# Optimization experiments

Hardware: AMD Instinct MI355X
Metric: run time of the kernel (lower is better)

## Reference

```python
import jax, jax.numpy as jnp
import numpy as np

B, IN_DIM, D, C = 8192, 2048, 1024, 1000


def setup_inputs() -> dict:
    key = jax.random.key(0)
    k1, k2, k3 = jax.random.split(key, 3)
    x = jax.random.normal(k1, (B, IN_DIM), dtype=jnp.float32)
    W_enc = jax.random.normal(k2, (IN_DIM, D), dtype=jnp.float32) * 0.02
    b_enc = jnp.zeros((D,), dtype=jnp.float32)
    prototypes = jax.random.normal(k3, (C, D), dtype=jnp.float32)
    return {"x": x, "W_enc": W_enc, "b_enc": b_enc, "prototypes": prototypes}


def reference(x, W_enc, b_enc, prototypes):
    # Encoder features Z: [B, D] (stand-in for model.forward_encoder)
    Z = x @ W_enc + b_enc
    # MSELoss(Z[i], proto[j]) = mean over D of squared diff
    # = (||z||^2 + ||p||^2 - 2 z.p) / D  -- avoids [B, C, D] intermediate
    z2 = jnp.sum(Z * Z, axis=-1, keepdims=True)          # [B, 1]
    p2 = jnp.sum(prototypes * prototypes, axis=-1)[None]  # [1, C]
    cross = jnp.einsum("bd,cd->bc", Z, prototypes)        # [B, C]
    mse = (z2 + p2 - 2.0 * cross) / jnp.asarray(Z.shape[-1], Z.dtype)
    return -mse
```

## Files before the change

### kernel.cpp

```cpp
#include <hip/hip_runtime.h>

#define B_ROWS 8192
#define IN_DIM 2048
#define D_DIM  1024
#define C_CLS  1000

typedef __attribute__((ext_vector_type(8))) short   bf16x8;
typedef __attribute__((ext_vector_type(4))) float   f32x4;

__device__ __forceinline__ unsigned short f2b(float f) {
    unsigned int u = __builtin_bit_cast(unsigned int, f);
    u = u + 0x7fffu + ((u >> 16) & 1u);
    return (unsigned short)(u >> 16);
}
__device__ __forceinline__ void g2lds16(const void* g, void* l) {
    __builtin_amdgcn_global_load_lds(
        (const __attribute__((address_space(1))) unsigned int*)g,
        (__attribute__((address_space(3))) unsigned int*)l,
        16, 0, 0);
}

__global__ __launch_bounds__(256) void k_pre(const float* __restrict__ W,
                                             const float* __restrict__ P,
                                             const float* __restrict__ x,
                                             unsigned short* __restrict__ Wt,
                                             unsigned short* __restrict__ Pb,
                                             unsigned short* __restrict__ xb,
                                             float* __restrict__ p2) {
    const int tid = threadIdx.x;
    if (blockIdx.x >= 3072) {
        const size_t i = (((size_t)blockIdx.x - 3072) * 256 + tid) * 8;
        float4 v0 = *(const float4*)(x + i);
        float4 v1 = *(const float4*)(x + i + 4);
        bf16x8 h;
        h[0] = (short)f2b(v0.x); h[1] = (short)f2b(v0.y);
        h[2] = (short)f2b(v0.z); h[3] = (short)f2b(v0.w);
        h[4] = (short)f2b(v1.x); h[5] = (short)f2b(v1.y);
        h[6] = (short)f2b(v1.z); h[7] = (short)f2b(v1.w);
        *(bf16x8*)(xb + i) = h;
    } else if (blockIdx.x < 2048) {
        __shared__ float t[32][33];
        const int tx = tid & 31, ty = tid >> 5;
        const int kb = (blockIdx.x & 63) * 32;
        const int nb = (blockIdx.x >> 6) * 32;
#pragma unroll
        for (int j = 0; j < 4; ++j)
            t[ty + 8 * j][tx] = W[(size_t)(kb + ty + 8 * j) * D_DIM + nb + tx];
        __syncthreads();
#pragma unroll
        for (int j = 0; j < 4; ++j)
            Wt[(size_t)(nb + ty + 8 * j) * IN_DIM + kb + tx] = f2b(t[tx][ty + 8 * j]);
    } else {
        const int c = blockIdx.x - 2048;
        float s = 0.f;
        if (c < C_CLS) {
            float4 v = *((const float4*)(P + (size_t)c * D_DIM) + tid);
            s = v.x * v.x + v.y * v.y + v.z * v.z + v.w * v.w;
            ushort4 h; h.x = f2b(v.x); h.y = f2b(v.y); h.z = f2b(v.z); h.w = f2b(v.w);
            *((ushort4*)(Pb + (size_t)c * D_DIM) + tid) = h;
        } else {
            ushort4 h; h.x = 0; h.y = 0; h.z = 0; h.w = 0;
            *((ushort4*)(Pb + (size_t)c * D_DIM) + tid) = h;
        }
#pragma unroll
        for (int o = 32; o > 0; o >>= 1) s += __shfl_down(s, o);
        __shared__ float red[4];
        if ((tid & 63) == 0) red[tid >> 6] = s;
        __syncthreads();
        if (tid == 0) p2[c] = red[0] + red[1] + red[2] + red[3];
    }
}

template <int MODE>
__global__ __launch_bounds__(512, 2) void k_gemm8(
    const unsigned short* __restrict__ Ab,
    const unsigned short* __restrict__ Bt,
    const float* __restrict__ bias,
    const float* __restrict__ z2p_in,
    const float* __restrict__ p2,
    unsigned short* __restrict__ Zout,
    float* __restrict__ z2p_out,
    float* __restrict__ Out) {
    constexpr int K  = (MODE == 0) ? IN_DIM : D_DIM;
    constexpr int NT = K / 64;
    constexpr unsigned ASZ = 256 * 64 * 2;
    constexpr unsigned BSZ = 128 * 64 * 2;
    extern __shared__ char lds[];
    char* pa0 = lds;            char* pa1 = lds + ASZ;  char* pa2 = lds + 2 * ASZ;
    char* pb0 = lds + 3 * ASZ;  char* pb1 = pb0 + BSZ;  char* pb2 = pb0 + 2 * BSZ;
    float* z2loc = (float*)(lds + 3 * (ASZ + BSZ));

    const int tid  = threadIdx.x;
    const int wave = tid >> 6, lane = tid & 63;
    const int lo = lane & 15, hi = lane >> 4;
    const int wm = wave >> 1, wn = wave & 1;

    const int swz = ((blockIdx.x & 7) << 5) + (blockIdx.x >> 3);
    const int bm = swz >> 3, bn = swz & 7;
    const int rowbase = bm * 256, colbase = bn * 128;

    const int srow   = lane >> 3;
    const int gchunk = (lane & 7) ^ (srow & 7);

    auto STAGE_A = [&](char* dst, int kt, int i) {
        const int s = i * 8 + wave;
        g2lds16(Ab + (size_t)(rowbase + s * 8 + srow) * K + kt * 64 + gchunk * 8,
                dst + s * 1024);
    };
    auto STAGE_B = [&](char* dst, int kt, int i) {
        const int s = i * 8 + wave;
        g2lds16(Bt + (size_t)(colbase + s * 8 + srow) * K + kt * 64 + gchunk * 8,
                dst + s * 1024);
    };

    f32x4 acc[4][4];
#pragma unroll
    for (int m = 0; m < 4; ++m)
#pragma unroll
        for (int n = 0; n < 4; ++n) acc[m][n] = (f32x4){0.f, 0.f, 0.f, 0.f};

    if constexpr (MODE == 1) {
        if (tid < 256) {
            float s = 0.f;
#pragma unroll
            for (int j = 0; j < 16; ++j) s += z2p_in[j * B_ROWS + rowbase + tid];
            z2loc[tid] = s;
        }
    }
#pragma unroll
    for (int i = 0; i < 4; ++i) STAGE_A(pa0, 0, i);
    STAGE_B(pb0, 0, 0); STAGE_B(pb0, 0, 1);
#pragma unroll
    for (int i = 0; i < 4; ++i) STAGE_A(pa1, 1, i);
    STAGE_B(pb1, 1, 0); STAGE_B(pb1, 1, 1);
    asm volatile("s_waitcnt vmcnt(6) lgkmcnt(0)" ::: "memory");
    __builtin_amdgcn_s_barrier();

    auto COMPUTE = [&]() {
#pragma unroll
        for (int ks = 0; ks < 2; ++ks) {
            bf16x8 af[4], bfr[4];
#pragma unroll
            for (int m = 0; m < 4; ++m) {
                const int row = wm * 64 + m * 16 + lo;
                unsigned addr = (unsigned)(row * 128 + ks * 64 + hi * 16)
                              ^ (unsigned)((lo & 7) << 4);
                af[m] = *(const bf16x8*)(pa0 + addr);
            }
#pragma unroll
            for (int n = 0; n < 4; ++n) {
                const int row = wn * 64 + n * 16 + lo;
                unsigned addr = (unsigned)(row * 128 + ks * 64 + hi * 16)
                              ^ (unsigned)((lo & 7) << 4);
                bfr[n] = *(const bf16x8*)(pb0 + addr);
            }
            __builtin_amdgcn_s_setprio(1);
#pragma unroll
            for (int m = 0; m < 4; ++m)
#pragma unroll
                for (int n = 0; n < 4; ++n)
                    acc[m][n] = __builtin_amdgcn_mfma_f32_16x16x32_bf16(
                        af[m], bfr[n], acc[m][n], 0, 0, 0);
            __builtin_amdgcn_s_setprio(0);
        }
    };

    for (int t = 0; t < NT; ++t) {
        const bool stg = (t < NT - 2);
        if (stg) {
#pragma unroll
            for (int i = 0; i < 4; ++i) STAGE_A(pa2, t + 2, i);
            STAGE_B(pb2, t + 2, 0); STAGE_B(pb2, t + 2, 1);
        }
        COMPUTE();
        if (t < NT - 1) {
            if (stg) asm volatile("s_waitcnt vmcnt(6)" ::: "memory");
            else     asm volatile("s_waitcnt vmcnt(0)" ::: "memory");
            __builtin_amdgcn_s_barrier();
            char* ta = pa0; pa0 = pa1; pa1 = pa2; pa2 = ta;
            char* tb = pb0; pb0 = pb1; pb1 = pb2; pb2 = tb;
        }
    }

    if constexpr (MODE == 0) {
        float bv[4];
#pragma unroll
        for (int n = 0; n < 4; ++n) bv[n] = bias[colbase + wn * 64 + n * 16 + lo];
#pragma unroll
        for (int m = 0; m < 4; ++m)
#pragma unroll
            for (int r = 0; r < 4; ++r) {
                const int rg = rowbase + wm * 64 + m * 16 + hi * 4 + r;
                float s = 0.f;
#pragma unroll
                for (int n = 0; n < 4; ++n) {
                    const float zf = acc[m][n][r] + bv[n];
                    Zout[(size_t)rg * D_DIM + colbase + wn * 64 + n * 16 + lo] = f2b(zf);
                    s += zf * zf;
                }
                s += __shfl_xor(s, 1); s += __shfl_xor(s, 2);
                s += __shfl_xor(s, 4); s += __shfl_xor(s, 8);
                if (lo == 0) z2p_out[(size_t)(bn * 2 + wn) * B_ROWS + rg] = s;
            }
    } else {
        float p2v[4];
#pragma unroll
        for (int n = 0; n < 4; ++n) p2v[n] = p2[colbase + wn * 64 + n * 16 + lo];
#pragma unroll
        for (int m = 0; m < 4; ++m)
#pragma unroll
            for (int r = 0; r < 4; ++r) {
                const int rl = wm * 64 + m * 16 + hi * 4 + r;
                const int rg = rowbase + rl;
                const float zv = z2loc[rl];
#pragma unroll
                for (int n = 0; n < 4; ++n) {
                    const int cg = colbase + wn * 64 + n * 16 + lo;
                    if (cg < C_CLS)
                        Out[(size_t)rg * C_CLS + cg] =
                            (2.f * acc[m][n][r] - zv - p2v[n]) * (1.f / 1024.f);
                }
            }
    }
}

extern "C" void kernel_launch(void* const* d_in, const int* in_sizes, int n_in,
                              void* d_out, int out_size, void* d_ws, size_t ws_size,
                              hipStream_t stream) {
    const float* x = (const float*)d_in[0];
    const float* W = (const float*)d_in[1];
    const float* b = (const float*)d_in[2];
    const float* P = (const float*)d_in[3];
    float* out = (float*)d_out;

    char* ws = (char*)d_ws;
    unsigned short* Wt  = (unsigned short*)(ws);
    unsigned short* Pb  = (unsigned short*)(ws + (4  << 20));
    unsigned short* Zb  = (unsigned short*)(ws + (6  << 20));
    float*          p2  = (float*)(ws + (22 << 20) + (64 << 10));
    float*          z2p = (float*)(ws + (22 << 20) + (128 << 10));
    unsigned short* xb  = (unsigned short*)(ws + (23 << 20));

    const unsigned lds_bytes = 3 * (256 * 64 * 2 + 128 * 64 * 2) + 1024;

    k_pre<<<dim3(11264), dim3(256), 0, stream>>>(W, P, x, Wt, Pb, xb, p2);
    k_gemm8<0><<<dim3(256), dim3(512), lds_bytes, stream>>>(
        xb, Wt, b, nullptr, nullptr, Zb, z2p, nullptr);
    k_gemm8<1><<<dim3(256), dim3(512), lds_bytes, stream>>>(
        Zb, Pb, nullptr, z2p, p2, nullptr, nullptr, out);
}
```

Baseline: 80.53 us.

## Split MFMA main loop into four quadrant phases interleaving LDS reads and staging

Restructures the per-tile compute loop into four quadrant phases. Each phase reads a small set of A/B fragments from LDS, issues part of the global-to-LDS staging for tile t+2, then runs eight MFMAs. Barriers separate the phases so waves stay in lockstep, in the style of ping-pong scheduling. The aim is to overlap LDS reads and global loads with MFMA issue and to lower register pressure. The cost is several extra barriers per tile, plus some B fragments reloaded from LDS.

```diff
diff --git a/kernel.cpp b/kernel.cpp
--- a/kernel.cpp
+++ b/kernel.cpp
@@ -136,43 +136,88 @@
     asm volatile("s_waitcnt vmcnt(6) lgkmcnt(0)" ::: "memory");
     __builtin_amdgcn_s_barrier();
 
-    auto COMPUTE = [&]() {
-#pragma unroll
-        for (int ks = 0; ks < 2; ++ks) {
-            bf16x8 af[4], bfr[4];
-#pragma unroll
-            for (int m = 0; m < 4; ++m) {
-                const int row = wm * 64 + m * 16 + lo;
-                unsigned addr = (unsigned)(row * 128 + ks * 64 + hi * 16)
-                              ^ (unsigned)((lo & 7) << 4);
-                af[m] = *(const bf16x8*)(pa0 + addr);
-            }
-#pragma unroll
-            for (int n = 0; n < 4; ++n) {
-                const int row = wn * 64 + n * 16 + lo;
-                unsigned addr = (unsigned)(row * 128 + ks * 64 + hi * 16)
-                              ^ (unsigned)((lo & 7) << 4);
-                bfr[n] = *(const bf16x8*)(pb0 + addr);
-            }
-            __builtin_amdgcn_s_setprio(1);
-#pragma unroll
-            for (int m = 0; m < 4; ++m)
-#pragma unroll
-                for (int n = 0; n < 4; ++n)
-                    acc[m][n] = __builtin_amdgcn_mfma_f32_16x16x32_bf16(
-                        af[m], bfr[n], acc[m][n], 0, 0, 0);
-            __builtin_amdgcn_s_setprio(0);
-        }
+    auto RD_A = [&](int mrow, int ks) -> bf16x8 {
+        const int row = wm * 64 + mrow * 16 + lo;
+        unsigned addr = (unsigned)(row * 128 + ks * 64 + hi * 16)
+                      ^ (unsigned)((lo & 7) << 4);
+        return *(const bf16x8*)(pa0 + addr);
+    };
+    auto RD_B = [&](int nrow, int ks) -> bf16x8 {
+        const int row = wn * 64 + nrow * 16 + lo;
+        unsigned addr = (unsigned)(row * 128 + ks * 64 + hi * 16)
+                      ^ (unsigned)((lo & 7) << 4);
+        return *(const bf16x8*)(pb0 + addr);
     };
 
     for (int t = 0; t < NT; ++t) {
         const bool stg = (t < NT - 2);
-        if (stg) {
-#pragma unroll
-            for (int i = 0; i < 4; ++i) STAGE_A(pa2, t + 2, i);
-            STAGE_B(pb2, t + 2, 0); STAGE_B(pb2, t + 2, 1);
-        }
-        COMPUTE();
+        bf16x8 a0k0, a0k1, a1k0, a1k1;
+        bf16x8 b0k0, b0k1, b1k0, b1k1;
+
+        a0k0 = RD_A(0, 0); a0k1 = RD_A(0, 1);
+        a1k0 = RD_A(1, 0); a1k1 = RD_A(1, 1);
+        b0k0 = RD_B(0, 0); b0k1 = RD_B(0, 1);
+        b1k0 = RD_B(1, 0); b1k1 = RD_B(1, 1);
+        if (stg) { STAGE_A(pa2, t + 2, 0); STAGE_A(pa2, t + 2, 1); }
+        __builtin_amdgcn_s_barrier();
+        __builtin_amdgcn_s_setprio(1);
+        acc[0][0] = __builtin_amdgcn_mfma_f32_16x16x32_bf16(a0k0, b0k0, acc[0][0], 0, 0, 0);
+        acc[0][1] = __builtin_amdgcn_mfma_f32_16x16x32_bf16(a0k0, b1k0, acc[0][1], 0, 0, 0);
+        acc[1][0] = __builtin_amdgcn_mfma_f32_16x16x32_bf16(a1k0, b0k0, acc[1][0], 0, 0, 0);
+        acc[1][1] = __builtin_amdgcn_mfma_f32_16x16x32_bf16(a1k0, b1k0, acc[1][1], 0, 0, 0);
+        acc[0][0] = __builtin_amdgcn_mfma_f32_16x16x32_bf16(a0k1, b0k1, acc[0][0], 0, 0, 0);
+        acc[0][1] = __builtin_amdgcn_mfma_f32_16x16x32_bf16(a0k1, b1k1, acc[0][1], 0, 0, 0);
+        acc[1][0] = __builtin_amdgcn_mfma_f32_16x16x32_bf16(a1k1, b0k1, acc[1][0], 0, 0, 0);
+        acc[1][1] = __builtin_amdgcn_mfma_f32_16x16x32_bf16(a1k1, b1k1, acc[1][1], 0, 0, 0);
+        __builtin_amdgcn_s_setprio(0);
+        __builtin_amdgcn_s_barrier();
+
+        b0k0 = RD_B(2, 0); b0k1 = RD_B(2, 1);
+        b1k0 = RD_B(3, 0); b1k1 = RD_B(3, 1);
+        if (stg) { STAGE_A(pa2, t + 2, 2); STAGE_A(pa2, t + 2, 3); }
+        __builtin_amdgcn_s_barrier();
+        __builtin_amdgcn_s_setprio(1);
+        acc[0][2] = __builtin_amdgcn_mfma_f32_16x16x32_bf16(a0k0, b0k0, acc[0][2], 0, 0, 0);
+        acc[0][3] = __builtin_amdgcn_mfma_f32_16x16x32_bf16(a0k0, b1k0, acc[0][3], 0, 0, 0);
+        acc[1][2] = __builtin_amdgcn_mfma_f32_16x16x32_bf16(a1k0, b0k0, acc[1][2], 0, 0, 0);
+        acc[1][3] = __builtin_amdgcn_mfma_f32_16x16x32_bf16(a1k0, b1k0, acc[1][3], 0, 0, 0);
+        acc[0][2] = __builtin_amdgcn_mfma_f32_16x16x32_bf16(a0k1, b0k1, acc[0][2], 0, 0, 0);
+        acc[0][3] = __builtin_amdgcn_mfma_f32_16x16x32_bf16(a0k1, b1k1, acc[0][3], 0, 0, 0);
+        acc[1][2] = __builtin_amdgcn_mfma_f32_16x16x32_bf16(a1k1, b0k1, acc[1][2], 0, 0, 0);
+        acc[1][3] = __builtin_amdgcn_mfma_f32_16x16x32_bf16(a1k1, b1k1, acc[1][3], 0, 0, 0);
+        __builtin_amdgcn_s_setprio(0);
+        __builtin_amdgcn_s_barrier();
+
+        a0k0 = RD_A(2, 0); a0k1 = RD_A(2, 1);
+        a1k0 = RD_A(3, 0); a1k1 = RD_A(3, 1);
+        if (stg) { STAGE_B(pb2, t + 2, 0); STAGE_B(pb2, t + 2, 1); }
+        __builtin_amdgcn_s_barrier();
+        __builtin_amdgcn_s_setprio(1);
+        acc[2][2] = __builtin_amdgcn_mfma_f32_16x16x32_bf16(a0k0, b0k0, acc[2][2], 0, 0, 0);
+        acc[2][3] = __builtin_amdgcn_mfma_f32_16x16x32_bf16(a0k0, b1k0, acc[2][3], 0, 0, 0);
+        acc[3][2] = __builtin_amdgcn_mfma_f32_16x16x32_bf16(a1k0, b0k0, acc[3][2], 0, 0, 0);
+        acc[3][3] = __builtin_amdgcn_mfma_f32_16x16x32_bf16(a1k0, b1k0, acc[3][3], 0, 0, 0);
+        acc[2][2] = __builtin_amdgcn_mfma_f32_16x16x32_bf16(a0k1, b0k1, acc[2][2], 0, 0, 0);
+        acc[2][3] = __builtin_amdgcn_mfma_f32_16x16x32_bf16(a0k1, b1k1, acc[2][3], 0, 0, 0);
+        acc[3][2] = __builtin_amdgcn_mfma_f32_16x16x32_bf16(a1k1, b0k1, acc[3][2], 0, 0, 0);
+        acc[3][3] = __builtin_amdgcn_mfma_f32_16x16x32_bf16(a1k1, b1k1, acc[3][3], 0, 0, 0);
+        __builtin_amdgcn_s_setprio(0);
+        __builtin_amdgcn_s_barrier();
+
+        b0k0 = RD_B(0, 0); b0k1 = RD_B(0, 1);
+        b1k0 = RD_B(1, 0); b1k1 = RD_B(1, 1);
+        __builtin_amdgcn_s_barrier();
+        __builtin_amdgcn_s_setprio(1);
+        acc[2][0] = __builtin_amdgcn_mfma_f32_16x16x32_bf16(a0k0, b0k0, acc[2][0], 0, 0, 0);
+        acc[2][1] = __builtin_amdgcn_mfma_f32_16x16x32_bf16(a0k0, b1k0, acc[2][1], 0, 0, 0);
+        acc[3][0] = __builtin_amdgcn_mfma_f32_16x16x32_bf16(a1k0, b0k0, acc[3][0], 0, 0, 0);
+        acc[3][1] = __builtin_amdgcn_mfma_f32_16x16x32_bf16(a1k0, b1k0, acc[3][1], 0, 0, 0);
+        acc[2][0] = __builtin_amdgcn_mfma_f32_16x16x32_bf16(a0k1, b0k1, acc[2][0], 0, 0, 0);
+        acc[2][1] = __builtin_amdgcn_mfma_f32_16x16x32_bf16(a0k1, b1k1, acc[2][1], 0, 0, 0);
+        acc[3][0] = __builtin_amdgcn_mfma_f32_16x16x32_bf16(a1k1, b0k1, acc[3][0], 0, 0, 0);
+        acc[3][1] = __builtin_amdgcn_mfma_f32_16x16x32_bf16(a1k1, b1k1, acc[3][1], 0, 0, 0);
+        __builtin_amdgcn_s_setprio(0);
+
         if (t < NT - 1) {
             if (stg) asm volatile("s_waitcnt vmcnt(6)" ::: "memory");
             else     asm volatile("s_waitcnt vmcnt(0)" ::: "memory");
```

New measurement: 83.73 us. +4.0%, slower.

## Shrink GEMM block tile to 128x128 with four waves and double buffering

Applied to the files above, without the earlier changes.

Both GEMM kernels move from 256x128 tiles run by 512-thread blocks with a three-stage LDS pipeline to 128x128 tiles run by 256-thread blocks with two-stage buffering. The launch grid doubles to 512 blocks and the LDS footprint per block shrinks. The aim is more blocks in flight per CU and less LDS pressure. In exchange, each tile is reused less, so more global traffic is needed. Each iteration also waits on vmcnt(0), which removes the deeper prefetch overlap.

```diff
diff --git a/kernel.cpp b/kernel.cpp
--- a/kernel.cpp
+++ b/kernel.cpp
@@ -72,7 +72,7 @@
 }
 
 template <int MODE>
-__global__ __launch_bounds__(512, 2) void k_gemm8(
+__global__ __launch_bounds__(256, 2) void k_gemm(
     const unsigned short* __restrict__ Ab,
     const unsigned short* __restrict__ Bt,
     const float* __restrict__ bias,
@@ -83,34 +83,40 @@
     float* __restrict__ Out) {
     constexpr int K  = (MODE == 0) ? IN_DIM : D_DIM;
     constexpr int NT = K / 64;
-    constexpr unsigned ASZ = 256 * 64 * 2;
+    constexpr unsigned ASZ = 128 * 64 * 2;
     constexpr unsigned BSZ = 128 * 64 * 2;
     extern __shared__ char lds[];
-    char* pa0 = lds;            char* pa1 = lds + ASZ;  char* pa2 = lds + 2 * ASZ;
-    char* pb0 = lds + 3 * ASZ;  char* pb1 = pb0 + BSZ;  char* pb2 = pb0 + 2 * BSZ;
-    float* z2loc = (float*)(lds + 3 * (ASZ + BSZ));
+    char* pa0 = lds;             char* pa1 = lds + ASZ;
+    char* pb0 = lds + 2 * ASZ;   char* pb1 = pb0 + BSZ;
+    float* z2loc = (float*)(lds + 2 * ASZ + 2 * BSZ);
 
     const int tid  = threadIdx.x;
     const int wave = tid >> 6, lane = tid & 63;
     const int lo = lane & 15, hi = lane >> 4;
     const int wm = wave >> 1, wn = wave & 1;
 
-    const int swz = ((blockIdx.x & 7) << 5) + (blockIdx.x >> 3);
+    const int swz = (blockIdx.x & 7) * 64 + (blockIdx.x >> 3);
     const int bm = swz >> 3, bn = swz & 7;
-    const int rowbase = bm * 256, colbase = bn * 128;
+    const int rowbase = bm * 128, colbase = bn * 128;
 
     const int srow   = lane >> 3;
     const int gchunk = (lane & 7) ^ (srow & 7);
 
-    auto STAGE_A = [&](char* dst, int kt, int i) {
-        const int s = i * 8 + wave;
-        g2lds16(Ab + (size_t)(rowbase + s * 8 + srow) * K + kt * 64 + gchunk * 8,
-                dst + s * 1024);
+    auto STAGE_A = [&](char* dst, int kt) {
+#pragma unroll
+        for (int i = 0; i < 4; ++i) {
+            const int s = i * 4 + wave;
+            g2lds16(Ab + (size_t)(rowbase + s * 8 + srow) * K + kt * 64 + gchunk * 8,
+                    dst + s * 1024);
+        }
     };
-    auto STAGE_B = [&](char* dst, int kt, int i) {
-        const int s = i * 8 + wave;
-        g2lds16(Bt + (size_t)(colbase + s * 8 + srow) * K + kt * 64 + gchunk * 8,
-                dst + s * 1024);
+    auto STAGE_B = [&](char* dst, int kt) {
+#pragma unroll
+        for (int i = 0; i < 4; ++i) {
+            const int s = i * 4 + wave;
+            g2lds16(Bt + (size_t)(colbase + s * 8 + srow) * K + kt * 64 + gchunk * 8,
+                    dst + s * 1024);
+        }
     };
 
     f32x4 acc[4][4];
@@ -120,20 +126,16 @@
         for (int n = 0; n < 4; ++n) acc[m][n] = (f32x4){0.f, 0.f, 0.f, 0.f};
 
     if constexpr (MODE == 1) {
-        if (tid < 256) {
+        if (tid < 128) {
             float s = 0.f;
 #pragma unroll
             for (int j = 0; j < 16; ++j) s += z2p_in[j * B_ROWS + rowbase + tid];
             z2loc[tid] = s;
         }
     }
-#pragma unroll
-    for (int i = 0; i < 4; ++i) STAGE_A(pa0, 0, i);
-    STAGE_B(pb0, 0, 0); STAGE_B(pb0, 0, 1);
-#pragma unroll
-    for (int i = 0; i < 4; ++i) STAGE_A(pa1, 1, i);
-    STAGE_B(pb1, 1, 0); STAGE_B(pb1, 1, 1);
-    asm volatile("s_waitcnt vmcnt(6) lgkmcnt(0)" ::: "memory");
+    STAGE_A(pa0, 0);
+    STAGE_B(pb0, 0);
+    asm volatile("s_waitcnt vmcnt(0) lgkmcnt(0)" ::: "memory");
     __builtin_amdgcn_s_barrier();
 
     auto COMPUTE = [&]() {
@@ -166,19 +168,17 @@
     };
 
     for (int t = 0; t < NT; ++t) {
-        const bool stg = (t < NT - 2);
-        if (stg) {
-#pragma unroll
-            for (int i = 0; i < 4; ++i) STAGE_A(pa2, t + 2, i);
-            STAGE_B(pb2, t + 2, 0); STAGE_B(pb2, t + 2, 1);
+        const bool nx = (t + 1 < NT);
+        if (nx) {
+            STAGE_A(pa1, t + 1);
+            STAGE_B(pb1, t + 1);
         }
         COMPUTE();
-        if (t < NT - 1) {
-            if (stg) asm volatile("s_waitcnt vmcnt(6)" ::: "memory");
-            else     asm volatile("s_waitcnt vmcnt(0)" ::: "memory");
+        if (nx) {
+            asm volatile("s_waitcnt vmcnt(0)" ::: "memory");
             __builtin_amdgcn_s_barrier();
-            char* ta = pa0; pa0 = pa1; pa1 = pa2; pa2 = ta;
-            char* tb = pb0; pb0 = pb1; pb1 = pb2; pb2 = tb;
+            char* ta = pa0; pa0 = pa1; pa1 = ta;
+            char* tb = pb0; pb0 = pb1; pb1 = tb;
         }
     }
 
@@ -241,11 +241,12 @@
     float*          z2p = (float*)(ws + (22 << 20) + (128 << 10));
     unsigned short* xb  = (unsigned short*)(ws + (23 << 20));
 
-    const unsigned lds_bytes = 3 * (256 * 64 * 2 + 128 * 64 * 2) + 1024;
+    const unsigned lds0 = 4 * (128 * 64 * 2);
+    const unsigned lds1 = lds0 + 512;
 
     k_pre<<<dim3(11264), dim3(256), 0, stream>>>(W, P, x, Wt, Pb, xb, p2);
-    k_gemm8<0><<<dim3(256), dim3(512), lds_bytes, stream>>>(
+    k_gemm<0><<<dim3(512), dim3(256), lds0, stream>>>(
         xb, Wt, b, nullptr, nullptr, Zb, z2p, nullptr);
-    k_gemm8<1><<<dim3(256), dim3(512), lds_bytes, stream>>>(
+    k_gemm<1><<<dim3(512), dim3(256), lds1, stream>>>(
         Zb, Pb, nullptr, z2p, p2, nullptr, nullptr, out);
 }
```

After: 81.53 us. Within noise of the previous version (+1.2%).
